# Optimization experiments

Hardware: AMD Instinct MI355X
Metric: run time of the kernel (lower is better)

## Reference

```python
import jax, jax.numpy as jnp
import numpy as np

B, T, V, D, H, L = 64, 256, 65, 384, 6, 6
HD = D // H
FF = 4 * D
EPS = 1e-5


def _layernorm(x, w, b):
    m = x.mean(-1, keepdims=True)
    v = ((x - m) ** 2).mean(-1, keepdims=True)
    return (x - m) / jnp.sqrt(v + EPS) * w + b


def setup_inputs() -> dict:
    key = jax.random.key(0)
    ks = jax.random.split(key, 20)
    s = lambda k, shape, scale=0.02: jax.random.normal(k, shape, dtype=jnp.float32) * scale
    inp = {
        'idx': jax.random.randint(ks[0], (B, T), 0, V),
        'tok_emb': s(ks[1], (V, D)),
        'pos_emb': s(ks[2], (T, D)),
        'ln1_w': jnp.ones((L, D), jnp.float32),
        'ln1_b': jnp.zeros((L, D), jnp.float32),
        'wq': s(ks[3], (L, H, D, HD)),
        'wk': s(ks[4], (L, H, D, HD)),
        'wv': s(ks[5], (L, H, D, HD)),
        'proj_w': s(ks[6], (L, D, D)),
        'proj_b': jnp.zeros((L, D), jnp.float32),
        'ln2_w': jnp.ones((L, D), jnp.float32),
        'ln2_b': jnp.zeros((L, D), jnp.float32),
        'ff_w1': s(ks[7], (L, D, FF)),
        'ff_b1': jnp.zeros((L, FF), jnp.float32),
        'ff_w2': s(ks[8], (L, FF, D)),
        'ff_b2': jnp.zeros((L, D), jnp.float32),
        'lnf_w': jnp.ones((D,), jnp.float32),
        'lnf_b': jnp.zeros((D,), jnp.float32),
        'head_w': s(ks[9], (D, V)),
        'head_b': jnp.zeros((V,), jnp.float32),
    }
    return inp


def reference(idx, tok_emb, pos_emb, ln1_w, ln1_b, wq, wk, wv, proj_w, proj_b,
              ln2_w, ln2_b, ff_w1, ff_b1, ff_w2, ff_b2, lnf_w, lnf_b, head_w, head_b):
    t = idx.shape[1]
    x = tok_emb[idx] + pos_emb[:t]  # [B,T,D]
    causal = jnp.tril(jnp.ones((t, t), bool))
    scale = D ** -0.5  # NOTE: original scales by n_embd**-0.5, not head_size
    for l in range(L):
        h = _layernorm(x, ln1_w[l], ln1_b[l])
        q = jnp.einsum('btd,hde->bhte', h, wq[l])
        k = jnp.einsum('btd,hde->bhte', h, wk[l])
        v = jnp.einsum('btd,hde->bhte', h, wv[l])
        wei = jnp.einsum('bhte,bhse->bhts', q, k) * scale
        wei = jnp.where(causal, wei, -jnp.inf)
        wei = jax.nn.softmax(wei, axis=-1)
        o = jnp.einsum('bhts,bhse->bhte', wei, v)
        o = o.transpose(0, 2, 1, 3).reshape(x.shape[0], t, D)  # concat heads
        x = x + o @ proj_w[l] + proj_b[l]
        h2 = _layernorm(x, ln2_w[l], ln2_b[l])
        x = x + jnp.maximum(h2 @ ff_w1[l] + ff_b1[l], 0.0) @ ff_w2[l] + ff_b2[l]
    x = _layernorm(x, lnf_w, lnf_b)
    logits = x @ head_w + head_b  # [B,T,V]
    return logits
```

## Files before the change

### kernel.cpp

```cpp
#include <hip/hip_runtime.h>
#include <hip/hip_bf16.h>
#include <math.h>

#define BB   64
#define TT   256
#define VV   65
#define DD   384
#define HH   6
#define HDD  64
#define LL   6
#define FFD  1536
#define BT   (BB * TT)
#define EPSL 1e-5f
#define SCALE 0.05103103630798287f

using bf16x8 = __attribute__((ext_vector_type(8))) short;
using f32x4  = __attribute__((ext_vector_type(4))) float;

__device__ __forceinline__ short f2bf(float f) {
    __hip_bfloat16 h = __float2bfloat16(f);
    return *reinterpret_cast<short*>(&h);
}
__device__ __forceinline__ float bf2f(short s) {
    union { unsigned u; float f; } c;
    c.u = ((unsigned)(unsigned short)s) << 16;
    return c.f;
}

__device__ __forceinline__ void load_lds16(const void* g, void* lds_base) {
    __builtin_amdgcn_global_load_lds(
        (const __attribute__((address_space(1))) void*)g,
        (__attribute__((address_space(3))) void*)lds_base,
        16, 0, 0);
}

__global__ __launch_bounds__(256) void embed_k(const int* __restrict__ idx,
                                               const float* __restrict__ tok,
                                               const float* __restrict__ pos,
                                               short* __restrict__ x) {
    int i = blockIdx.x * 256 + threadIdx.x;
    int bt = i / 48;
    int g  = i - bt * 48;
    int t  = bt & (TT - 1);
    const float4* tp = (const float4*)tok + (size_t)idx[bt] * 96 + g * 2;
    const float4* pp = (const float4*)pos + (size_t)t * 96 + g * 2;
    float4 a0 = tp[0], a1 = tp[1], p0 = pp[0], p1 = pp[1];
    bf16x8 o;
    o[0] = f2bf(a0.x + p0.x); o[1] = f2bf(a0.y + p0.y);
    o[2] = f2bf(a0.z + p0.z); o[3] = f2bf(a0.w + p0.w);
    o[4] = f2bf(a1.x + p1.x); o[5] = f2bf(a1.y + p1.y);
    o[6] = f2bf(a1.z + p1.z); o[7] = f2bf(a1.w + p1.w);
    *reinterpret_cast<bf16x8*>(x + (size_t)bt * DD + g * 8) = o;
}

__global__ __launch_bounds__(256) void ln_k(const short* __restrict__ in,
                                            const float* __restrict__ w,
                                            const float* __restrict__ b,
                                            short* __restrict__ out) {
    int row  = blockIdx.x * 4 + (threadIdx.x >> 6);
    int lane = threadIdx.x & 63;
    const unsigned* pu = (const unsigned*)(in + (size_t)row * DD);
    unsigned u0 = pu[lane], u1 = pu[lane + 64], u2 = pu[lane + 128];
    float v00 = bf2f((short)(u0 & 0xffff)), v01 = bf2f((short)(u0 >> 16));
    float v10 = bf2f((short)(u1 & 0xffff)), v11 = bf2f((short)(u1 >> 16));
    float v20 = bf2f((short)(u2 & 0xffff)), v21 = bf2f((short)(u2 >> 16));
    float s = v00 + v01 + v10 + v11 + v20 + v21;
#pragma unroll
    for (int off = 32; off; off >>= 1) s += __shfl_xor(s, off);
    float mean = s * (1.0f / DD);
    float d00 = v00 - mean, d01 = v01 - mean, d10 = v10 - mean,
          d11 = v11 - mean, d20 = v20 - mean, d21 = v21 - mean;
    float s2 = d00*d00 + d01*d01 + d10*d10 + d11*d11 + d20*d20 + d21*d21;
#pragma unroll
    for (int off = 32; off; off >>= 1) s2 += __shfl_xor(s2, off);
    float rstd = rsqrtf(s2 * (1.0f / DD) + EPSL);
    int c0 = lane * 2, c1 = c0 + 128, c2 = c0 + 256;
    unsigned* po = (unsigned*)(out + (size_t)row * DD);
    unsigned r0 = (unsigned)(unsigned short)f2bf(d00 * rstd * w[c0] + b[c0]) |
                  ((unsigned)(unsigned short)f2bf(d01 * rstd * w[c0+1] + b[c0+1]) << 16);
    unsigned r1 = (unsigned)(unsigned short)f2bf(d10 * rstd * w[c1] + b[c1]) |
                  ((unsigned)(unsigned short)f2bf(d11 * rstd * w[c1+1] + b[c1+1]) << 16);
    unsigned r2 = (unsigned)(unsigned short)f2bf(d20 * rstd * w[c2] + b[c2]) |
                  ((unsigned)(unsigned short)f2bf(d21 * rstd * w[c2+1] + b[c2+1]) << 16);
    po[lane] = r0; po[lane + 64] = r1; po[lane + 128] = r2;
}

__global__ __launch_bounds__(256) void wconv_k(const float* __restrict__ W,
                                               short* __restrict__ Wt,
                                               int K, int N, int Npad) {
    __shared__ float tile[32][33];
    W  += (size_t)blockIdx.z * K * N;
    Wt += (size_t)blockIdx.z * Npad * K;
    const int t  = threadIdx.x;
    const int c  = t & 31;
    const int r8 = t >> 5;
    const int k0 = blockIdx.y * 32;
    const int n0 = blockIdx.x * 32;
#pragma unroll
    for (int p = 0; p < 4; ++p) {
        int kk = r8 + 8 * p;
        int n  = n0 + c;
        tile[kk][c] = (n < N) ? W[(size_t)(k0 + kk) * N + n] : 0.f;
    }
    __syncthreads();
#pragma unroll
    for (int p = 0; p < 4; ++p) {
        int nl = r8 + 8 * p;
        Wt[(size_t)(n0 + nl) * K + k0 + c] = f2bf(tile[c][nl]);
    }
}

__global__ __launch_bounds__(256) void qkvconv_k(const float* __restrict__ wq,
                                                 const float* __restrict__ wk,
                                                 const float* __restrict__ wv,
                                                 short* __restrict__ Wt) {
    int tid = blockIdx.x * 256 + threadIdx.x;
    int e  = tid & 63;
    int k  = (tid >> 6) % 384;
    int r2 = (tid >> 6) / 384;
    int h  = r2 % 6;
    int r3 = r2 / 6;
    int part = r3 % 3;
    int l  = r3 / 3;
    const float* src = (part == 0) ? wq : (part == 1) ? wk : wv;
    float v = src[(((size_t)l * 6 + h) * 384 + k) * 64 + e];
    Wt[((size_t)l * 1152 + part * 384 + h * 64 + e) * 384 + k] = f2bf(v);
}

__global__ __launch_bounds__(256, 6) void gemm128_k(
    const short* __restrict__ A,
    const short* __restrict__ Bt,
    const float* __restrict__ bias,
    const short* __restrict__ res16,
    float* __restrict__ out32,
    short* __restrict__ out16,
    int M, int K, int ldC, int Nmax, int relu) {
    __shared__ short As[128 * 64];
    __shared__ short Bs[64 * 64];
    const int t  = threadIdx.x;
    const int w  = t >> 6;
    const int l  = t & 63;

    const int gx  = gridDim.x;
    const int nwg = gx * gridDim.y;
    const int lin = blockIdx.y * gx + blockIdx.x;
    const int cpx = nwg >> 3;
    const int swz = (lin & 7) * cpx + (lin >> 3);
    const int m0 = (swz / gx) * 128;
    const int n0 = (swz % gx) * 64;

    const int wr = w >> 1, wc = w & 1;
    const int fr = l & 15, fq = l >> 4;

    int arow[4], acol[4];
#pragma unroll
    for (int qi = 0; qi < 4; ++qi) {
        int r = (w * 4 + qi) * 8 + (l >> 3);
        arow[qi] = r;
        acol[qi] = (l & 7) ^ (r & 7);
    }
    int brow[2], bcol[2];
#pragma unroll
    for (int qi = 0; qi < 2; ++qi) {
        int r = (w * 2 + qi) * 8 + (l >> 3);
        brow[qi] = r;
        bcol[qi] = (l & 7) ^ (r & 7);
    }

    f32x4 acc[4][2];
#pragma unroll
    for (int i = 0; i < 4; ++i)
#pragma unroll
        for (int j = 0; j < 2; ++j) acc[i][j] = (f32x4)(0.0f);

    const int nt = K >> 6;

    for (int tk = 0; tk < nt; ++tk) {
        const int k0 = tk << 6;
#pragma unroll
        for (int qi = 0; qi < 4; ++qi)
            load_lds16(A + (size_t)(m0 + arow[qi]) * K + k0 + acol[qi] * 8,
                       (char*)As + (w * 4 + qi) * 1024);
#pragma unroll
        for (int qi = 0; qi < 2; ++qi)
            load_lds16(Bt + (size_t)(n0 + brow[qi]) * K + k0 + bcol[qi] * 8,
                       (char*)Bs + (w * 2 + qi) * 1024);
        asm volatile("s_waitcnt vmcnt(0)" ::: "memory");
        __syncthreads();

        __builtin_amdgcn_s_setprio(1);
#pragma unroll
        for (int ks = 0; ks < 2; ++ks) {
            const int kc = ks * 4 + fq;
            bf16x8 af[4], bfv[2];
#pragma unroll
            for (int mf = 0; mf < 4; ++mf) {
                int ar = wr * 64 + mf * 16 + fr;
                af[mf] = *reinterpret_cast<const bf16x8*>(
                    (const char*)As + ar * 128 + ((kc ^ (ar & 7)) << 4));
            }
#pragma unroll
            for (int nf = 0; nf < 2; ++nf) {
                int br = wc * 32 + nf * 16 + fr;
                bfv[nf] = *reinterpret_cast<const bf16x8*>(
                    (const char*)Bs + br * 128 + ((kc ^ (br & 7)) << 4));
            }
#pragma unroll
            for (int mf = 0; mf < 4; ++mf)
#pragma unroll
                for (int nf = 0; nf < 2; ++nf)
                    acc[mf][nf] = __builtin_amdgcn_mfma_f32_16x16x32_bf16(
                        af[mf], bfv[nf], acc[mf][nf], 0, 0, 0);
        }
        __builtin_amdgcn_s_setprio(0);
        __syncthreads();
    }

#pragma unroll
    for (int mf = 0; mf < 4; ++mf) {
#pragma unroll
        for (int nf = 0; nf < 2; ++nf) {
            int n = n0 + wc * 32 + nf * 16 + fr;
            if (n < Nmax) {
#pragma unroll
                for (int j = 0; j < 4; ++j) {
                    int m = m0 + wr * 64 + mf * 16 + fq * 4 + j;
                    float v = acc[mf][nf][j];
                    if (bias)   v += bias[n];
                    if (res16)  v += bf2f(res16[(size_t)m * ldC + n]);
                    if (relu)   v = fmaxf(v, 0.f);
                    if (out32)  out32[(size_t)m * ldC + n] = v;
                    if (out16)  out16[(size_t)m * ldC + n] = f2bf(v);
                }
            }
        }
    }
}

__global__ __launch_bounds__(256) void attn_mfma_k(const short* __restrict__ qkv,
                                                   short* __restrict__ o) {
    __shared__ short Vt[16384];
    __shared__ short Pw[4][4096];

    const int hh = blockIdx.x;
    const int bb = blockIdx.y;
    const int t  = threadIdx.x;
    const int w  = t >> 6;
    const int lane = t & 63;
    const int fr = lane & 15, fq = lane >> 4;
    const int bt0 = bb * TT;

    {
        const int r0 = (t & 127) * 2;
        const int dbase = (t >> 7) * 32;
        const short* v0 = qkv + (size_t)(bt0 + r0) * 1152 + 768 + hh * 64 + dbase;
        short a0[32], a1[32];
#pragma unroll
        for (int i = 0; i < 4; ++i) {
            *(bf16x8*)(a0 + i * 8) = *(const bf16x8*)(v0 + i * 8);
            *(bf16x8*)(a1 + i * 8) = *(const bf16x8*)(v0 + 1152 + i * 8);
        }
#pragma unroll
        for (int i = 0; i < 32; ++i) {
            int d = dbase + i;
            int byte = (d * 512 + r0 * 2) ^ ((d & 7) << 4);
            unsigned int pk = (unsigned int)(unsigned short)a0[i] |
                              ((unsigned int)(unsigned short)a1[i] << 16);
            *(unsigned int*)((char*)Vt + byte) = pk;
        }
    }
    __syncthreads();

    char* PwW = (char*)Pw[w];

    bf16x8 qb[4][2];
#pragma unroll
    for (int nf = 0; nf < 4; ++nf)
#pragma unroll
        for (int ks = 0; ks < 2; ++ks)
            qb[nf][ks] = *(const bf16x8*)(qkv + (size_t)(bt0 + w * 64 + nf * 16 + fr) * 1152 +
                                          hh * 64 + ks * 32 + fq * 8);

    f32x4 o_acc[4][4];
#pragma unroll
    for (int i = 0; i < 4; ++i)
#pragma unroll
        for (int j = 0; j < 4; ++j) o_acc[i][j] = (f32x4)(0.0f);
    float m_run[4], l_run[4];
#pragma unroll
    for (int nf = 0; nf < 4; ++nf) { m_run[nf] = -1e30f; l_run[nf] = 0.f; }

    for (int kt = 0; kt <= w; ++kt) {
        bf16x8 ak[4][2];
#pragma unroll
        for (int mf = 0; mf < 4; ++mf)
#pragma unroll
            for (int ks = 0; ks < 2; ++ks)
                ak[mf][ks] = *(const bf16x8*)(qkv + (size_t)(bt0 + kt * 64 + mf * 16 + fr) * 1152 +
                                              384 + hh * 64 + ks * 32 + fq * 8);

        f32x4 s[4][4];
#pragma unroll
        for (int i = 0; i < 4; ++i)
#pragma unroll
            for (int j = 0; j < 4; ++j) s[i][j] = (f32x4)(0.0f);
#pragma unroll
        for (int ks = 0; ks < 2; ++ks)
#pragma unroll
            for (int mf = 0; mf < 4; ++mf)
#pragma unroll
                for (int nf = 0; nf < 4; ++nf)
                    s[mf][nf] = __builtin_amdgcn_mfma_f32_16x16x32_bf16(
                        ak[mf][ks], qb[nf][ks], s[mf][nf], 0, 0, 0);

        const bool diag = (kt == w);
#pragma unroll
        for (int mf = 0; mf < 4; ++mf)
#pragma unroll
            for (int nf = 0; nf < 4; ++nf)
#pragma unroll
                for (int j = 0; j < 4; ++j) {
                    float v = s[mf][nf][j] * SCALE;
                    if (diag && (mf * 16 + fq * 4 + j > nf * 16 + fr)) v = -1e30f;
                    s[mf][nf][j] = v;
                }

        float fac[4];
#pragma unroll
        for (int nf = 0; nf < 4; ++nf) {
            float mx = -1e30f;
#pragma unroll
            for (int mf = 0; mf < 4; ++mf)
#pragma unroll
                for (int j = 0; j < 4; ++j) mx = fmaxf(mx, s[mf][nf][j]);
            mx = fmaxf(mx, __shfl_xor(mx, 16));
            mx = fmaxf(mx, __shfl_xor(mx, 32));
            float mnew = fmaxf(m_run[nf], mx);
            fac[nf] = __expf(m_run[nf] - mnew);
            m_run[nf] = mnew;
        }

#pragma unroll
        for (int nf = 0; nf < 4; ++nf) {
            float ps = 0.f;
#pragma unroll
            for (int mf = 0; mf < 4; ++mf)
#pragma unroll
                for (int j = 0; j < 4; ++j) {
                    float p = __expf(s[mf][nf][j] - m_run[nf]);
                    s[mf][nf][j] = p;
                    ps += p;
                }
            ps += __shfl_xor(ps, 16);
            ps += __shfl_xor(ps, 32);
            l_run[nf] = l_run[nf] * fac[nf] + ps;
        }

#pragma unroll
        for (int mf = 0; mf < 4; ++mf)
#pragma unroll
            for (int nf = 0; nf < 4; ++nf) {
                unsigned long long pk =
                    (unsigned long long)(unsigned short)f2bf(s[mf][nf][0]) |
                    ((unsigned long long)(unsigned short)f2bf(s[mf][nf][1]) << 16) |
                    ((unsigned long long)(unsigned short)f2bf(s[mf][nf][2]) << 32) |
                    ((unsigned long long)(unsigned short)f2bf(s[mf][nf][3]) << 48);
                int q = nf * 16 + fr;
                int byte = (q * 128 + mf * 32 + fq * 8) ^ ((q & 7) << 4);
                *(unsigned long long*)(PwW + byte) = pk;
            }

#pragma unroll
        for (int j = 0; j < 4; ++j) {
            int src = (lane & 48) + ((lane & 48) >> 2) + j;
#pragma unroll
            for (int mo = 0; mo < 4; ++mo) {
                float f = __shfl(fac[mo], src);
#pragma unroll
                for (int df = 0; df < 4; ++df) o_acc[mo][df][j] *= f;
            }
        }

        bf16x8 ap[4][2], bv[4][2];
#pragma unroll
        for (int mo = 0; mo < 4; ++mo)
#pragma unroll
            for (int ks = 0; ks < 2; ++ks) {
                int byte = ((mo * 16 + fr) * 128 + ks * 64 + fq * 16) ^ ((fr & 7) << 4);
                ap[mo][ks] = *(const bf16x8*)(PwW + byte);
            }
#pragma unroll
        for (int df = 0; df < 4; ++df)
#pragma unroll
            for (int ks = 0; ks < 2; ++ks) {
                int byte = ((df * 16 + fr) * 512 + kt * 128 + ks * 64 + fq * 16) ^ ((fr & 7) << 4);
                bv[df][ks] = *(const bf16x8*)((const char*)Vt + byte);
            }
#pragma unroll
        for (int ks = 0; ks < 2; ++ks)
#pragma unroll
            for (int mo = 0; mo < 4; ++mo)
#pragma unroll
                for (int df = 0; df < 4; ++df)
                    o_acc[mo][df] = __builtin_amdgcn_mfma_f32_16x16x32_bf16(
                        ap[mo][ks], bv[df][ks], o_acc[mo][df], 0, 0, 0);
    }

    float linv[4];
#pragma unroll
    for (int nf = 0; nf < 4; ++nf) linv[nf] = 1.0f / l_run[nf];
#pragma unroll
    for (int j = 0; j < 4; ++j) {
        int src = (lane & 48) + ((lane & 48) >> 2) + j;
#pragma unroll
        for (int mo = 0; mo < 4; ++mo) {
            float li = __shfl(linv[mo], src);
#pragma unroll
            for (int df = 0; df < 4; ++df) {
                float val = o_acc[mo][df][j] * li;
                o[(size_t)(bt0 + w * 64 + mo * 16 + fq * 4 + j) * DD + hh * 64 + df * 16 + fr] =
                    f2bf(val);
            }
        }
    }
}

extern "C" void kernel_launch(void* const* d_in, const int* in_sizes, int n_in,
                              void* d_out, int out_size, void* d_ws, size_t ws_size,
                              hipStream_t stream) {
    const int*   idx     = (const int*)d_in[0];
    const float* tok_emb = (const float*)d_in[1];
    const float* pos_emb = (const float*)d_in[2];
    const float* ln1_w   = (const float*)d_in[3];
    const float* ln1_b   = (const float*)d_in[4];
    const float* wq      = (const float*)d_in[5];
    const float* wk      = (const float*)d_in[6];
    const float* wv      = (const float*)d_in[7];
    const float* proj_w  = (const float*)d_in[8];
    const float* proj_b  = (const float*)d_in[9];
    const float* ln2_w   = (const float*)d_in[10];
    const float* ln2_b   = (const float*)d_in[11];
    const float* ff_w1   = (const float*)d_in[12];
    const float* ff_b1   = (const float*)d_in[13];
    const float* ff_w2   = (const float*)d_in[14];
    const float* ff_b2   = (const float*)d_in[15];
    const float* lnf_w   = (const float*)d_in[16];
    const float* lnf_b   = (const float*)d_in[17];
    const float* head_w  = (const float*)d_in[18];
    const float* head_b  = (const float*)d_in[19];
    float* out = (float*)d_out;

    char* p = (char*)d_ws;
    short* x16    = (short*)p;  p += (size_t)BT * DD * 2;
    short* qkv16  = (short*)p;  p += (size_t)BT * 1152 * 2;
    short* h16    = (short*)p;  p += (size_t)BT * DD * 2;
    short* o16    = (short*)p;  p += (size_t)BT * DD * 2;
    short* ff16   = (short*)p;  p += (size_t)BT * FFD * 2;
    short* wqkvT  = (short*)p;  p += (size_t)LL * 1152 * 384 * 2;
    short* projT  = (short*)p;  p += (size_t)LL * 384 * 384 * 2;
    short* ff1T   = (short*)p;  p += (size_t)LL * 1536 * 384 * 2;
    short* ff2T   = (short*)p;  p += (size_t)LL * 384 * 1536 * 2;
    short* headT  = (short*)p;  p += (size_t)128 * 384 * 2;

    const dim3 blk(256);

    qkvconv_k<<<dim3(2654208 / 256), blk, 0, stream>>>(wq, wk, wv, wqkvT);
    wconv_k<<<dim3(12, 12, 6), blk, 0, stream>>>(proj_w, projT, 384, 384, 384);
    wconv_k<<<dim3(48, 12, 6), blk, 0, stream>>>(ff_w1, ff1T, 384, 1536, 1536);
    wconv_k<<<dim3(12, 48, 6), blk, 0, stream>>>(ff_w2, ff2T, 1536, 384, 384);
    wconv_k<<<dim3(4, 12, 1), blk, 0, stream>>>(head_w, headT, 384, 65, 128);

    embed_k<<<dim3((BT * 48) / 256), blk, 0, stream>>>(idx, tok_emb, pos_emb, x16);

    const dim3 gLN(BT / 4);
    const dim3 gAttn(HH, BB);
    const dim3 gQKV(1152 / 64, BT / 128);
    const dim3 gD(384 / 64, BT / 128);
    const dim3 gFF(1536 / 64, BT / 128);
    const dim3 gHead(128 / 64, BT / 128);

    for (int l = 0; l < LL; ++l) {
        const size_t dOff = (size_t)l * DD;

        ln_k<<<gLN, blk, 0, stream>>>(x16, ln1_w + dOff, ln1_b + dOff, h16);

        gemm128_k<<<gQKV, blk, 0, stream>>>(h16, wqkvT + (size_t)l * 1152 * 384,
                                            nullptr, nullptr, nullptr, qkv16,
                                            BT, 384, 1152, 1152, 0);

        attn_mfma_k<<<gAttn, blk, 0, stream>>>(qkv16, o16);

        gemm128_k<<<gD, blk, 0, stream>>>(o16, projT + (size_t)l * 384 * 384,
                                          proj_b + dOff, x16, nullptr, x16,
                                          BT, 384, 384, 384, 0);

        ln_k<<<gLN, blk, 0, stream>>>(x16, ln2_w + dOff, ln2_b + dOff, h16);

        gemm128_k<<<gFF, blk, 0, stream>>>(h16, ff1T + (size_t)l * 1536 * 384,
                                           ff_b1 + (size_t)l * FFD, nullptr,
                                           nullptr, ff16,
                                           BT, 384, 1536, 1536, 1);

        gemm128_k<<<gD, blk, 0, stream>>>(ff16, ff2T + (size_t)l * 384 * 1536,
                                          ff_b2 + dOff, x16, nullptr, x16,
                                          BT, 1536, 384, 384, 0);
    }

    ln_k<<<gLN, blk, 0, stream>>>(x16, lnf_w, lnf_b, h16);
    gemm128_k<<<gHead, blk, 0, stream>>>(h16, headT, head_b, nullptr, out, nullptr,
                                         BT, 384, 65, 65, 0);
}
```

Measured before the change: 1.287 ms.

## Shrink GEMM tiles to 64x64 and balance causal attention with paired query tiles

The GEMM kernel now uses 64x64 output tiles instead of 128x64, doubling the number of workgroups and raising the occupancy hint. The attention kernel splits queries into 32-row tiles, and each wave handles one early and one late tile (w and 7-w) so causal work is even across waves. Previously the last wave did four times the work of the first. The cost is less data reuse per GEMM tile and more K-tile reloads in attention.

```diff
diff --git a/kernel.cpp b/kernel.cpp
--- a/kernel.cpp
+++ b/kernel.cpp
@@ -127,7 +127,7 @@
     Wt[((size_t)l * 1152 + part * 384 + h * 64 + e) * 384 + k] = f2bf(v);
 }
 
-__global__ __launch_bounds__(256, 6) void gemm128_k(
+__global__ __launch_bounds__(256, 8) void gemm64_k(
     const short* __restrict__ A,
     const short* __restrict__ Bt,
     const float* __restrict__ bias,
@@ -135,8 +135,8 @@
     float* __restrict__ out32,
     short* __restrict__ out16,
     int M, int K, int ldC, int Nmax, int relu) {
-    __shared__ short As[128 * 64];
-    __shared__ short Bs[64 * 64];
+    __shared__ short As[4096];
+    __shared__ short Bs[4096];
     const int t  = threadIdx.x;
     const int w  = t >> 6;
     const int l  = t & 63;
@@ -146,30 +146,25 @@
     const int lin = blockIdx.y * gx + blockIdx.x;
     const int cpx = nwg >> 3;
     const int swz = (lin & 7) * cpx + (lin >> 3);
-    const int m0 = (swz / gx) * 128;
+    const int m0 = (swz / gx) * 64;
     const int n0 = (swz % gx) * 64;
 
     const int wr = w >> 1, wc = w & 1;
     const int fr = l & 15, fq = l >> 4;
 
-    int arow[4], acol[4];
-#pragma unroll
-    for (int qi = 0; qi < 4; ++qi) {
-        int r = (w * 4 + qi) * 8 + (l >> 3);
-        arow[qi] = r;
-        acol[qi] = (l & 7) ^ (r & 7);
-    }
-    int brow[2], bcol[2];
+    int srow[2], scol[2];
 #pragma unroll
     for (int qi = 0; qi < 2; ++qi) {
-        int r = (w * 2 + qi) * 8 + (l >> 3);
-        brow[qi] = r;
-        bcol[qi] = (l & 7) ^ (r & 7);
-    }
-
-    f32x4 acc[4][2];
-#pragma unroll
-    for (int i = 0; i < 4; ++i)
+        int s = w * 2 + qi;
+        int r = s * 8 + (l >> 3);
+        int c = l & 7;
+        srow[qi] = r;
+        scol[qi] = c ^ (r & 7);
+    }
+
+    f32x4 acc[2][2];
+#pragma unroll
+    for (int i = 0; i < 2; ++i)
 #pragma unroll
         for (int j = 0; j < 2; ++j) acc[i][j] = (f32x4)(0.0f);
 
@@ -178,12 +173,12 @@
     for (int tk = 0; tk < nt; ++tk) {
         const int k0 = tk << 6;
 #pragma unroll
-        for (int qi = 0; qi < 4; ++qi)
-            load_lds16(A + (size_t)(m0 + arow[qi]) * K + k0 + acol[qi] * 8,
-                       (char*)As + (w * 4 + qi) * 1024);
-#pragma unroll
         for (int qi = 0; qi < 2; ++qi)
-            load_lds16(Bt + (size_t)(n0 + brow[qi]) * K + k0 + bcol[qi] * 8,
+            load_lds16(A + (size_t)(m0 + srow[qi]) * K + k0 + scol[qi] * 8,
+                       (char*)As + (w * 2 + qi) * 1024);
+#pragma unroll
+        for (int qi = 0; qi < 2; ++qi)
+            load_lds16(Bt + (size_t)(n0 + srow[qi]) * K + k0 + scol[qi] * 8,
                        (char*)Bs + (w * 2 + qi) * 1024);
         asm volatile("s_waitcnt vmcnt(0)" ::: "memory");
         __syncthreads();
@@ -192,10 +187,10 @@
 #pragma unroll
         for (int ks = 0; ks < 2; ++ks) {
             const int kc = ks * 4 + fq;
-            bf16x8 af[4], bfv[2];
-#pragma unroll
-            for (int mf = 0; mf < 4; ++mf) {
-                int ar = wr * 64 + mf * 16 + fr;
+            bf16x8 af[2], bfv[2];
+#pragma unroll
+            for (int mf = 0; mf < 2; ++mf) {
+                int ar = wr * 32 + mf * 16 + fr;
                 af[mf] = *reinterpret_cast<const bf16x8*>(
                     (const char*)As + ar * 128 + ((kc ^ (ar & 7)) << 4));
             }
@@ -206,7 +201,7 @@
                     (const char*)Bs + br * 128 + ((kc ^ (br & 7)) << 4));
             }
 #pragma unroll
-            for (int mf = 0; mf < 4; ++mf)
+            for (int mf = 0; mf < 2; ++mf)
 #pragma unroll
                 for (int nf = 0; nf < 2; ++nf)
                     acc[mf][nf] = __builtin_amdgcn_mfma_f32_16x16x32_bf16(
@@ -217,14 +212,14 @@
     }
 
 #pragma unroll
-    for (int mf = 0; mf < 4; ++mf) {
+    for (int mf = 0; mf < 2; ++mf) {
 #pragma unroll
         for (int nf = 0; nf < 2; ++nf) {
             int n = n0 + wc * 32 + nf * 16 + fr;
             if (n < Nmax) {
 #pragma unroll
                 for (int j = 0; j < 4; ++j) {
-                    int m = m0 + wr * 64 + mf * 16 + fq * 4 + j;
+                    int m = m0 + wr * 32 + mf * 16 + fq * 4 + j;
                     float v = acc[mf][nf][j];
                     if (bias)   v += bias[n];
                     if (res16)  v += bf2f(res16[(size_t)m * ldC + n]);
@@ -240,7 +235,7 @@
 __global__ __launch_bounds__(256) void attn_mfma_k(const short* __restrict__ qkv,
                                                    short* __restrict__ o) {
     __shared__ short Vt[16384];
-    __shared__ short Pw[4][4096];
+    __shared__ short Pw[4][2048];
 
     const int hh = blockIdx.x;
     const int bb = blockIdx.y;
@@ -273,153 +268,162 @@
 
     char* PwW = (char*)Pw[w];
 
-    bf16x8 qb[4][2];
-#pragma unroll
-    for (int nf = 0; nf < 4; ++nf)
-#pragma unroll
-        for (int ks = 0; ks < 2; ++ks)
-            qb[nf][ks] = *(const bf16x8*)(qkv + (size_t)(bt0 + w * 64 + nf * 16 + fr) * 1152 +
-                                          hh * 64 + ks * 32 + fq * 8);
-
-    f32x4 o_acc[4][4];
-#pragma unroll
-    for (int i = 0; i < 4; ++i)
-#pragma unroll
-        for (int j = 0; j < 4; ++j) o_acc[i][j] = (f32x4)(0.0f);
-    float m_run[4], l_run[4];
-#pragma unroll
-    for (int nf = 0; nf < 4; ++nf) { m_run[nf] = -1e30f; l_run[nf] = 0.f; }
-
-    for (int kt = 0; kt <= w; ++kt) {
-        bf16x8 ak[4][2];
-#pragma unroll
-        for (int mf = 0; mf < 4; ++mf)
+#pragma unroll
+    for (int grp = 0; grp < 2; ++grp) {
+        const int qt = grp ? (7 - w) : w;
+        const int q0 = qt * 32;
+        const int ktm = qt >> 1;
+
+        bf16x8 qb[2][2];
+#pragma unroll
+        for (int nf = 0; nf < 2; ++nf)
 #pragma unroll
             for (int ks = 0; ks < 2; ++ks)
-                ak[mf][ks] = *(const bf16x8*)(qkv + (size_t)(bt0 + kt * 64 + mf * 16 + fr) * 1152 +
-                                              384 + hh * 64 + ks * 32 + fq * 8);
-
-        f32x4 s[4][4];
-#pragma unroll
-        for (int i = 0; i < 4; ++i)
-#pragma unroll
-            for (int j = 0; j < 4; ++j) s[i][j] = (f32x4)(0.0f);
-#pragma unroll
-        for (int ks = 0; ks < 2; ++ks)
+                qb[nf][ks] = *(const bf16x8*)(qkv + (size_t)(bt0 + q0 + nf * 16 + fr) * 1152 +
+                                              hh * 64 + ks * 32 + fq * 8);
+
+        f32x4 o_acc[2][4];
+#pragma unroll
+        for (int i = 0; i < 2; ++i)
+#pragma unroll
+            for (int j = 0; j < 4; ++j) o_acc[i][j] = (f32x4)(0.0f);
+        float m_run[2] = {-1e30f, -1e30f};
+        float l_run[2] = {0.f, 0.f};
+
+        for (int kt = 0; kt <= ktm; ++kt) {
+            bf16x8 ak[4][2];
 #pragma unroll
             for (int mf = 0; mf < 4; ++mf)
 #pragma unroll
-                for (int nf = 0; nf < 4; ++nf)
-                    s[mf][nf] = __builtin_amdgcn_mfma_f32_16x16x32_bf16(
-                        ak[mf][ks], qb[nf][ks], s[mf][nf], 0, 0, 0);
-
-        const bool diag = (kt == w);
-#pragma unroll
-        for (int mf = 0; mf < 4; ++mf)
-#pragma unroll
-            for (int nf = 0; nf < 4; ++nf)
-#pragma unroll
-                for (int j = 0; j < 4; ++j) {
-                    float v = s[mf][nf][j] * SCALE;
-                    if (diag && (mf * 16 + fq * 4 + j > nf * 16 + fr)) v = -1e30f;
-                    s[mf][nf][j] = v;
+                for (int ks = 0; ks < 2; ++ks)
+                    ak[mf][ks] = *(const bf16x8*)(qkv +
+                        (size_t)(bt0 + kt * 64 + mf * 16 + fr) * 1152 +
+                        384 + hh * 64 + ks * 32 + fq * 8);
+
+            f32x4 s[4][2];
+#pragma unroll
+            for (int i = 0; i < 4; ++i)
+#pragma unroll
+                for (int j = 0; j < 2; ++j) s[i][j] = (f32x4)(0.0f);
+#pragma unroll
+            for (int ks = 0; ks < 2; ++ks)
+#pragma unroll
+                for (int mf = 0; mf < 4; ++mf)
+#pragma unroll
+                    for (int nf = 0; nf < 2; ++nf)
+                        s[mf][nf] = __builtin_amdgcn_mfma_f32_16x16x32_bf16(
+                            ak[mf][ks], qb[nf][ks], s[mf][nf], 0, 0, 0);
+
+            const bool diag = (kt == ktm);
+#pragma unroll
+            for (int mf = 0; mf < 4; ++mf)
+#pragma unroll
+                for (int nf = 0; nf < 2; ++nf)
+#pragma unroll
+                    for (int j = 0; j < 4; ++j) {
+                        float v = s[mf][nf][j] * SCALE;
+                        if (diag && (kt * 64 + mf * 16 + fq * 4 + j >
+                                     q0 + nf * 16 + fr)) v = -1e30f;
+                        s[mf][nf][j] = v;
+                    }
+
+            float fac[2];
+#pragma unroll
+            for (int nf = 0; nf < 2; ++nf) {
+                float mx = -1e30f;
+#pragma unroll
+                for (int mf = 0; mf < 4; ++mf)
+#pragma unroll
+                    for (int j = 0; j < 4; ++j) mx = fmaxf(mx, s[mf][nf][j]);
+                mx = fmaxf(mx, __shfl_xor(mx, 16));
+                mx = fmaxf(mx, __shfl_xor(mx, 32));
+                float mnew = fmaxf(m_run[nf], mx);
+                fac[nf] = __expf(m_run[nf] - mnew);
+                m_run[nf] = mnew;
+            }
+
+#pragma unroll
+            for (int nf = 0; nf < 2; ++nf) {
+                float ps = 0.f;
+#pragma unroll
+                for (int mf = 0; mf < 4; ++mf)
+#pragma unroll
+                    for (int j = 0; j < 4; ++j) {
+                        float p = __expf(s[mf][nf][j] - m_run[nf]);
+                        s[mf][nf][j] = p;
+                        ps += p;
+                    }
+                ps += __shfl_xor(ps, 16);
+                ps += __shfl_xor(ps, 32);
+                l_run[nf] = l_run[nf] * fac[nf] + ps;
+            }
+
+#pragma unroll
+            for (int mf = 0; mf < 4; ++mf)
+#pragma unroll
+                for (int nf = 0; nf < 2; ++nf) {
+                    unsigned long long pk =
+                        (unsigned long long)(unsigned short)f2bf(s[mf][nf][0]) |
+                        ((unsigned long long)(unsigned short)f2bf(s[mf][nf][1]) << 16) |
+                        ((unsigned long long)(unsigned short)f2bf(s[mf][nf][2]) << 32) |
+                        ((unsigned long long)(unsigned short)f2bf(s[mf][nf][3]) << 48);
+                    int q = nf * 16 + fr;
+                    int byte = (q * 128 + mf * 32 + fq * 8) ^ ((q & 7) << 4);
+                    *(unsigned long long*)(PwW + byte) = pk;
                 }
 
-        float fac[4];
-#pragma unroll
-        for (int nf = 0; nf < 4; ++nf) {
-            float mx = -1e30f;
-#pragma unroll
-            for (int mf = 0; mf < 4; ++mf)
-#pragma unroll
-                for (int j = 0; j < 4; ++j) mx = fmaxf(mx, s[mf][nf][j]);
-            mx = fmaxf(mx, __shfl_xor(mx, 16));
-            mx = fmaxf(mx, __shfl_xor(mx, 32));
-            float mnew = fmaxf(m_run[nf], mx);
-            fac[nf] = __expf(m_run[nf] - mnew);
-            m_run[nf] = mnew;
+#pragma unroll
+            for (int j = 0; j < 4; ++j) {
+                int src = (lane & 48) + ((lane & 48) >> 2) + j;
+#pragma unroll
+                for (int mo = 0; mo < 2; ++mo) {
+                    float f = __shfl(fac[mo], src);
+#pragma unroll
+                    for (int df = 0; df < 4; ++df) o_acc[mo][df][j] *= f;
+                }
+            }
+
+            bf16x8 ap[2][2], bv[4][2];
+#pragma unroll
+            for (int mo = 0; mo < 2; ++mo)
+#pragma unroll
+                for (int ks = 0; ks < 2; ++ks) {
+                    int byte = ((mo * 16 + fr) * 128 + ks * 64 + fq * 16) ^ ((fr & 7) << 4);
+                    ap[mo][ks] = *(const bf16x8*)(PwW + byte);
+                }
+#pragma unroll
+            for (int df = 0; df < 4; ++df)
+#pragma unroll
+                for (int ks = 0; ks < 2; ++ks) {
+                    int byte = ((df * 16 + fr) * 512 + kt * 128 + ks * 64 + fq * 16) ^
+                               ((fr & 7) << 4);
+                    bv[df][ks] = *(const bf16x8*)((const char*)Vt + byte);
+                }
+#pragma unroll
+            for (int ks = 0; ks < 2; ++ks)
+#pragma unroll
+                for (int mo = 0; mo < 2; ++mo)
+#pragma unroll
+                    for (int df = 0; df < 4; ++df)
+                        o_acc[mo][df] = __builtin_amdgcn_mfma_f32_16x16x32_bf16(
+                            ap[mo][ks], bv[df][ks], o_acc[mo][df], 0, 0, 0);
         }
 
-#pragma unroll
-        for (int nf = 0; nf < 4; ++nf) {
-            float ps = 0.f;
-#pragma unroll
-            for (int mf = 0; mf < 4; ++mf)
-#pragma unroll
-                for (int j = 0; j < 4; ++j) {
-                    float p = __expf(s[mf][nf][j] - m_run[nf]);
-                    s[mf][nf][j] = p;
-                    ps += p;
-                }
-            ps += __shfl_xor(ps, 16);
-            ps += __shfl_xor(ps, 32);
-            l_run[nf] = l_run[nf] * fac[nf] + ps;
-        }
-
-#pragma unroll
-        for (int mf = 0; mf < 4; ++mf)
-#pragma unroll
-            for (int nf = 0; nf < 4; ++nf) {
-                unsigned long long pk =
-                    (unsigned long long)(unsigned short)f2bf(s[mf][nf][0]) |
-                    ((unsigned long long)(unsigned short)f2bf(s[mf][nf][1]) << 16) |
-                    ((unsigned long long)(unsigned short)f2bf(s[mf][nf][2]) << 32) |
-                    ((unsigned long long)(unsigned short)f2bf(s[mf][nf][3]) << 48);
-                int q = nf * 16 + fr;
-                int byte = (q * 128 + mf * 32 + fq * 8) ^ ((q & 7) << 4);
-                *(unsigned long long*)(PwW + byte) = pk;
-            }
-
+        float linv[2];
+#pragma unroll
+        for (int nf = 0; nf < 2; ++nf) linv[nf] = 1.0f / l_run[nf];
 #pragma unroll
         for (int j = 0; j < 4; ++j) {
             int src = (lane & 48) + ((lane & 48) >> 2) + j;
 #pragma unroll
-            for (int mo = 0; mo < 4; ++mo) {
-                float f = __shfl(fac[mo], src);
-#pragma unroll
-                for (int df = 0; df < 4; ++df) o_acc[mo][df][j] *= f;
-            }
-        }
-
-        bf16x8 ap[4][2], bv[4][2];
-#pragma unroll
-        for (int mo = 0; mo < 4; ++mo)
-#pragma unroll
-            for (int ks = 0; ks < 2; ++ks) {
-                int byte = ((mo * 16 + fr) * 128 + ks * 64 + fq * 16) ^ ((fr & 7) << 4);
-                ap[mo][ks] = *(const bf16x8*)(PwW + byte);
-            }
-#pragma unroll
-        for (int df = 0; df < 4; ++df)
-#pragma unroll
-            for (int ks = 0; ks < 2; ++ks) {
-                int byte = ((df * 16 + fr) * 512 + kt * 128 + ks * 64 + fq * 16) ^ ((fr & 7) << 4);
-                bv[df][ks] = *(const bf16x8*)((const char*)Vt + byte);
-            }
-#pragma unroll
-        for (int ks = 0; ks < 2; ++ks)
-#pragma unroll
-            for (int mo = 0; mo < 4; ++mo)
-#pragma unroll
-                for (int df = 0; df < 4; ++df)
-                    o_acc[mo][df] = __builtin_amdgcn_mfma_f32_16x16x32_bf16(
-                        ap[mo][ks], bv[df][ks], o_acc[mo][df], 0, 0, 0);
-    }
-
-    float linv[4];
-#pragma unroll
-    for (int nf = 0; nf < 4; ++nf) linv[nf] = 1.0f / l_run[nf];
-#pragma unroll
-    for (int j = 0; j < 4; ++j) {
-        int src = (lane & 48) + ((lane & 48) >> 2) + j;
-#pragma unroll
-        for (int mo = 0; mo < 4; ++mo) {
-            float li = __shfl(linv[mo], src);
-#pragma unroll
-            for (int df = 0; df < 4; ++df) {
-                float val = o_acc[mo][df][j] * li;
-                o[(size_t)(bt0 + w * 64 + mo * 16 + fq * 4 + j) * DD + hh * 64 + df * 16 + fr] =
-                    f2bf(val);
+            for (int mo = 0; mo < 2; ++mo) {
+                float li = __shfl(linv[mo], src);
+#pragma unroll
+                for (int df = 0; df < 4; ++df) {
+                    float val = o_acc[mo][df][j] * li;
+                    o[(size_t)(bt0 + q0 + mo * 16 + fq * 4 + j) * DD +
+                      hh * 64 + df * 16 + fr] = f2bf(val);
+                }
             }
         }
     }
@@ -474,39 +478,39 @@
 
     const dim3 gLN(BT / 4);
     const dim3 gAttn(HH, BB);
-    const dim3 gQKV(1152 / 64, BT / 128);
-    const dim3 gD(384 / 64, BT / 128);
-    const dim3 gFF(1536 / 64, BT / 128);
-    const dim3 gHead(128 / 64, BT / 128);
+    const dim3 gQKV(1152 / 64, BT / 64);
+    const dim3 gD(384 / 64, BT / 64);
+    const dim3 gFF(1536 / 64, BT / 64);
+    const dim3 gHead(128 / 64, BT / 64);
 
     for (int l = 0; l < LL; ++l) {
         const size_t dOff = (size_t)l * DD;
 
         ln_k<<<gLN, blk, 0, stream>>>(x16, ln1_w + dOff, ln1_b + dOff, h16);
 
-        gemm128_k<<<gQKV, blk, 0, stream>>>(h16, wqkvT + (size_t)l * 1152 * 384,
-                                            nullptr, nullptr, nullptr, qkv16,
-                                            BT, 384, 1152, 1152, 0);
+        gemm64_k<<<gQKV, blk, 0, stream>>>(h16, wqkvT + (size_t)l * 1152 * 384,
+                                           nullptr, nullptr, nullptr, qkv16,
+                                           BT, 384, 1152, 1152, 0);
 
         attn_mfma_k<<<gAttn, blk, 0, stream>>>(qkv16, o16);
 
-        gemm128_k<<<gD, blk, 0, stream>>>(o16, projT + (size_t)l * 384 * 384,
-                                          proj_b + dOff, x16, nullptr, x16,
-                                          BT, 384, 384, 384, 0);
+        gemm64_k<<<gD, blk, 0, stream>>>(o16, projT + (size_t)l * 384 * 384,
+                                         proj_b + dOff, x16, nullptr, x16,
+                                         BT, 384, 384, 384, 0);
 
         ln_k<<<gLN, blk, 0, stream>>>(x16, ln2_w + dOff, ln2_b + dOff, h16);
 
-        gemm128_k<<<gFF, blk, 0, stream>>>(h16, ff1T + (size_t)l * 1536 * 384,
-                                           ff_b1 + (size_t)l * FFD, nullptr,
-                                           nullptr, ff16,
-                                           BT, 384, 1536, 1536, 1);
-
-        gemm128_k<<<gD, blk, 0, stream>>>(ff16, ff2T + (size_t)l * 384 * 1536,
-                                          ff_b2 + dOff, x16, nullptr, x16,
-                                          BT, 1536, 384, 384, 0);
+        gemm64_k<<<gFF, blk, 0, stream>>>(h16, ff1T + (size_t)l * 1536 * 384,
+                                          ff_b1 + (size_t)l * FFD, nullptr,
+                                          nullptr, ff16,
+                                          BT, 384, 1536, 1536, 1);
+
+        gemm64_k<<<gD, blk, 0, stream>>>(ff16, ff2T + (size_t)l * 384 * 1536,
+                                         ff_b2 + dOff, x16, nullptr, x16,
+                                         BT, 1536, 384, 384, 0);
     }
 
     ln_k<<<gLN, blk, 0, stream>>>(x16, lnf_w, lnf_b, h16);
-    gemm128_k<<<gHead, blk, 0, stream>>>(h16, headT, head_b, nullptr, out, nullptr,
-                                         BT, 384, 65, 65, 0);
-}
+    gemm64_k<<<gHead, blk, 0, stream>>>(h16, headT, head_b, nullptr, out, nullptr,
+                                        BT, 384, 65, 65, 0);
+}
```

After: 1.168 ms. -9.3%, faster.
